# Kernel optimization log

Hardware: AMD Instinct MI355X
Metric: run time of the kernel (lower is better)

## Reference

```python
import jax, jax.numpy as jnp
import numpy as np

B, S, E = 2, 2048, 1024
H = 16
D = E // H  # 64
SCALE = D ** -0.5


def setup_inputs() -> dict:
    key = jax.random.key(0)
    ks = jax.random.split(key, 9)
    w = lambda k: jax.random.normal(k, (E, E), dtype=jnp.float32) * 0.02
    b = lambda k: jax.random.normal(k, (E,), dtype=jnp.float32) * 0.02
    return {
        "hidden_states": jax.random.normal(ks[0], (B, S, E), dtype=jnp.float32),
        "q_w": w(ks[1]), "q_b": b(ks[2]),
        "k_w": w(ks[3]), "k_b": b(ks[4]),
        "v_w": w(ks[5]), "v_b": b(ks[6]),
        "o_w": w(ks[7]), "o_b": b(ks[8]),
    }


def reference(hidden_states, q_w, q_b, k_w, k_b, v_w, v_b, o_w, o_b):
    dtype = hidden_states.dtype
    # torch Linear: y = x @ W^T + b
    q = hidden_states @ q_w.T + q_b
    k = hidden_states @ k_w.T + k_b
    v = hidden_states @ v_w.T + v_b
    # [B,S,E] -> [B*H, S, D]
    split = lambda t: t.reshape(B, S, H, D).transpose(0, 2, 1, 3).reshape(B * H, S, D)
    q, k, v = split(q), split(k), split(v)
    # upcast_attention: fp32 QK^T, scaled (baddbmm with beta=0, no mask)
    scores = SCALE * jnp.einsum("bqd,bkd->bqk", q.astype(jnp.float32), k.astype(jnp.float32))
    # upcast_softmax: fp32 softmax over last dim (transpose_qk=False), cast back
    probs = jax.nn.softmax(scores, axis=-1).astype(dtype)
    # PV bmm, merge heads, out_proj (dropout p=0.0 -> identity)
    out = jnp.einsum("bqk,bkd->bqd", probs, v)
    out = out.reshape(B, H, S, D).transpose(0, 2, 1, 3).reshape(B, S, E)
    return out @ o_w.T + o_b
```

## Files before the change

kernel.cpp:

```cpp
#include <hip/hip_runtime.h>

typedef __bf16 bf16x8 __attribute__((ext_vector_type(8)));
typedef __bf16 bf16x4 __attribute__((ext_vector_type(4)));
typedef float  f32x4  __attribute__((ext_vector_type(4)));

#define CS 0.18033688011112042f

__device__ __forceinline__ float fast_exp2(float x) {
    return __builtin_amdgcn_exp2f(x);
}

__device__ __forceinline__ f32x4 MFMA(bf16x8 a, bf16x8 b, f32x4 c) {
    return __builtin_amdgcn_mfma_f32_16x16x32_bf16(a, b, c, 0, 0, 0);
}

__device__ __forceinline__ void ldsgcpy16(__bf16* lds, const __bf16* g) {
    __builtin_amdgcn_global_load_lds(
        (const __attribute__((address_space(1))) unsigned int*)g,
        (__attribute__((address_space(3))) unsigned int*)lds, 16, 0, 0);
}

__global__ __launch_bounds__(256) void cvt5_kernel(
    const float* __restrict__ s0, const float* __restrict__ s1,
    const float* __restrict__ s2, const float* __restrict__ s3,
    const float* __restrict__ s4,
    __bf16* __restrict__ d0, __bf16* __restrict__ d1, __bf16* __restrict__ d2,
    __bf16* __restrict__ d3, __bf16* __restrict__ d4)
{
    int blk = blockIdx.x;
    const float* src; __bf16* dst; int base;
    if (blk < 4096)      { src = s0; dst = d0; base = blk; }
    else if (blk < 5120) { src = s1; dst = d1; base = blk - 4096; }
    else if (blk < 6144) { src = s2; dst = d2; base = blk - 5120; }
    else if (blk < 7168) { src = s3; dst = d3; base = blk - 6144; }
    else                 { src = s4; dst = d4; base = blk - 7168; }
    int i = base * 1024 + threadIdx.x * 4;
    float4 v = *(const float4*)(src + i);
    bf16x4 o;
    o[0] = (__bf16)v.x; o[1] = (__bf16)v.y; o[2] = (__bf16)v.z; o[3] = (__bf16)v.w;
    *(bf16x4*)(dst + i) = o;
}

template <typename OutT, int BN>
__device__ __forceinline__ void gemm_core(const __bf16* __restrict__ A,
                                          const __bf16* __restrict__ W,
                                          const float* __restrict__ bias,
                                          OutT* __restrict__ C,
                                          int m0, int n0, bool vtrans)
{
    constexpr int NJ = BN / 32;
    __shared__ __bf16 As[128 * 64];
    __shared__ __bf16 Bs[BN * 64];

    const int tid  = threadIdx.x;
    const int lane = tid & 63;
    const int w    = tid >> 6;
    const int wm   = w & 1;
    const int wn   = w >> 1;
    const int s    = lane & 15;
    const int q    = lane >> 4;

    f32x4 acc[4][NJ];
#pragma unroll
    for (int i = 0; i < 4; i++)
#pragma unroll
        for (int j = 0; j < NJ; j++)
#pragma unroll
            for (int r = 0; r < 4; r++) acc[i][j][r] = 0.0f;

    for (int k0 = 0; k0 < 1024; k0 += 64) {
        __syncthreads();
#pragma unroll
        for (int t = 0; t < 4; t++) {
            int c   = tid + 256 * t;
            int row = c >> 3;
            int ccp = (c & 7) ^ (row & 7);
            ldsgcpy16(&As[c * 8], A + (size_t)(m0 + row) * 1024 + k0 + ccp * 8);
        }
#pragma unroll
        for (int t = 0; t < BN / 32; t++) {
            int c   = tid + 256 * t;
            int row = c >> 3;
            int ccp = (c & 7) ^ (row & 7);
            ldsgcpy16(&Bs[c * 8], W + (size_t)(n0 + row) * 1024 + k0 + ccp * 8);
        }
        __syncthreads();

#pragma unroll
        for (int kk = 0; kk < 2; kk++) {
            bf16x8 af[4], bf[NJ];
#pragma unroll
            for (int i = 0; i < 4; i++) {
                int row = wm * 64 + i * 16 + s;
                int idx = row * 64 + ((((kk << 2) + q) ^ (row & 7)) << 3);
                af[i] = *(const bf16x8*)&As[idx];
            }
#pragma unroll
            for (int j = 0; j < NJ; j++) {
                int row = wn * (BN / 2) + j * 16 + s;
                int idx = row * 64 + ((((kk << 2) + q) ^ (row & 7)) << 3);
                bf[j] = *(const bf16x8*)&Bs[idx];
            }
#pragma unroll
            for (int i = 0; i < 4; i++)
#pragma unroll
                for (int j = 0; j < NJ; j++)
                    acc[i][j] = MFMA(af[i], bf[j], acc[i][j]);
        }
    }

    if (vtrans) {
        __bf16* Vt = (__bf16*)C;
#pragma unroll
        for (int j = 0; j < NJ; j++) {
            int col = n0 + wn * (BN / 2) + j * 16 + s;
            int h   = col >> 6;
            int d   = col & 63;
            float bv = bias[col];
#pragma unroll
            for (int i = 0; i < 4; i++) {
                int rowb = m0 + wm * 64 + i * 16 + q * 4;
                int b    = rowb >> 11;
                int srow = rowb & 2047;
                bf16x4 pk;
#pragma unroll
                for (int r = 0; r < 4; r++) pk[r] = (__bf16)(acc[i][j][r] + bv);
                *(bf16x4*)&Vt[(size_t)((b * 16 + h) * 64 + d) * 2048 + srow] = pk;
            }
        }
    } else {
#pragma unroll
        for (int j = 0; j < NJ; j++) {
            int col = n0 + wn * (BN / 2) + j * 16 + s;
            float bv = bias[col];
#pragma unroll
            for (int i = 0; i < 4; i++) {
                int rowb = m0 + wm * 64 + i * 16 + q * 4;
#pragma unroll
                for (int r = 0; r < 4; r++) {
                    C[(size_t)(rowb + r) * 1024 + col] = (OutT)(acc[i][j][r] + bv);
                }
            }
        }
    }
}

__global__ __launch_bounds__(256) void gemm_qkv_kernel(
    const __bf16* __restrict__ X,
    const __bf16* __restrict__ Wq, const float* __restrict__ bq,
    const __bf16* __restrict__ Wk, const float* __restrict__ bk,
    const __bf16* __restrict__ Wv, const float* __restrict__ bv,
    __bf16* __restrict__ Q, __bf16* __restrict__ K, __bf16* __restrict__ Vt)
{
    int mt = blockIdx.x / 24;
    int nt = blockIdx.x % 24;
    int which = nt >> 3;
    const __bf16* W    = (which == 0) ? Wq : (which == 1) ? Wk : Wv;
    const float*  bias = (which == 0) ? bq : (which == 1) ? bk : bv;
    __bf16*       Out  = (which == 0) ? Q  : (which == 1) ? K  : Vt;
    gemm_core<__bf16, 128>(X, W, bias, Out, mt * 128, (nt & 7) * 128, which == 2);
}

__global__ __launch_bounds__(256) void gemm_o_kernel(
    const __bf16* __restrict__ Ain, const __bf16* __restrict__ Wo,
    const float* __restrict__ bo, float* __restrict__ Out)
{
    int mt = blockIdx.x >> 4;
    int nt = blockIdx.x & 15;
    gemm_core<float, 64>(Ain, Wo, bo, Out, mt * 128, nt * 64, false);
}

__global__ __launch_bounds__(256, 2) void attn_kernel(
    const __bf16* __restrict__ Q, const __bf16* __restrict__ K,
    const __bf16* __restrict__ Vt, __bf16* __restrict__ O)
{
    __shared__ __bf16 k_lds[128 * 64];
    __shared__ __bf16 vt_lds[64 * 128];
    __shared__ __bf16 p_lds[4 * 32 * 128];

    const int bh = blockIdx.x >> 4;
    const int qt = blockIdx.x & 15;
    const int b  = bh >> 4;
    const int h  = bh & 15;

    const int tid  = threadIdx.x;
    const int lane = tid & 63;
    const int w    = tid >> 6;
    const int s    = lane & 15;
    const int q    = lane >> 4;

    bf16x8 aq[2][2];
#pragma unroll
    for (int i = 0; i < 2; i++)
#pragma unroll
        for (int kd = 0; kd < 2; kd++) {
            int row = qt * 128 + w * 32 + i * 16 + s;
            aq[i][kd] = *(const bf16x8*)(Q + (size_t)(b * 2048 + row) * 1024 +
                                         h * 64 + kd * 32 + q * 8);
        }

    f32x4 acc_o[2][4];
    float lst[2][4];
#pragma unroll
    for (int i = 0; i < 2; i++)
#pragma unroll
        for (int r = 0; r < 4; r++) {
            lst[i][r] = 0.0f;
#pragma unroll
            for (int jd = 0; jd < 4; jd++) acc_o[i][jd][r] = 0.0f;
        }

    const int pbase = w * 32 * 128;

    bf16x8 kpre[4], vpre[4];
#pragma unroll
    for (int t = 0; t < 4; t++) {
        int c = tid + 256 * t;
        int krow = c >> 3, cc = c & 7;
        kpre[t] = *(const bf16x8*)(K + (size_t)(b * 2048 + krow) * 1024 +
                                   h * 64 + cc * 8);
        int d = c >> 4, ck = c & 15;
        vpre[t] = *(const bf16x8*)(Vt + (size_t)(bh * 64 + d) * 2048 + ck * 8);
    }

    for (int kc = 0; kc < 16; kc++) {
        __syncthreads();
#pragma unroll
        for (int t = 0; t < 4; t++) {
            int c = tid + 256 * t;
            int krow = c >> 3, cc = c & 7;
            int rho  = ((krow & 7) << 4) | (krow >> 3);
            *(bf16x8*)&k_lds[rho * 64 + ((cc ^ (rho & 7)) << 3)] = kpre[t];
            int d = c >> 4, ck = c & 15;
            *(bf16x8*)&vt_lds[(d * 16 + (ck ^ (d & 7))) << 3] = vpre[t];
        }
        __syncthreads();

        int kb2 = ((kc + 1) & 15) * 128;
#pragma unroll
        for (int t = 0; t < 4; t++) {
            int c = tid + 256 * t;
            int krow = c >> 3, cc = c & 7;
            kpre[t] = *(const bf16x8*)(K + (size_t)(b * 2048 + kb2 + krow) * 1024 +
                                       h * 64 + cc * 8);
            int d = c >> 4, ck = c & 15;
            vpre[t] = *(const bf16x8*)(Vt + (size_t)(bh * 64 + d) * 2048 + kb2 + ck * 8);
        }

        f32x4 sc[2][8];
#pragma unroll
        for (int i = 0; i < 2; i++)
#pragma unroll
            for (int j = 0; j < 8; j++)
#pragma unroll
                for (int r = 0; r < 4; r++) sc[i][j][r] = 0.0f;
#pragma unroll
        for (int kd = 0; kd < 2; kd++) {
#pragma unroll
            for (int j = 0; j < 8; j++) {
                int row = j * 16 + s;
                int idx = row * 64 + ((((kd << 2) + q) ^ (row & 7)) << 3);
                bf16x8 bf = *(const bf16x8*)&k_lds[idx];
                sc[0][j] = MFMA(aq[0][kd], bf, sc[0][j]);
                sc[1][j] = MFMA(aq[1][kd], bf, sc[1][j]);
            }
        }

#pragma unroll
        for (int i = 0; i < 2; i++)
#pragma unroll
            for (int r = 0; r < 4; r++) {
                int prow = i * 16 + q * 4 + r;
                bf16x8 pk;
                float rsum = 0.0f;
#pragma unroll
                for (int j = 0; j < 8; j++) {
                    float p = fast_exp2(sc[i][j][r] * CS);
                    rsum += p;
                    pk[j] = (__bf16)p;
                }
                lst[i][r] += rsum;
                int chunkp = s ^ (prow & 15);
                *(bf16x8*)&p_lds[pbase + prow * 128 + (chunkp << 3)] = pk;
            }

#pragma unroll
        for (int kk = 0; kk < 4; kk++) {
            bf16x8 ap[2];
#pragma unroll
            for (int i = 0; i < 2; i++) {
                int prow = i * 16 + s;
                int chunkr = ((kk << 2) + q) ^ s;
                ap[i] = *(const bf16x8*)&p_lds[pbase + prow * 128 + (chunkr << 3)];
            }
#pragma unroll
            for (int jd = 0; jd < 4; jd++) {
                int d    = jd * 16 + s;
                int vidx = (d * 16 + (((kk << 2) + q) ^ (d & 7))) << 3;
                bf16x8 bv = *(const bf16x8*)&vt_lds[vidx];
                acc_o[0][jd] = MFMA(ap[0], bv, acc_o[0][jd]);
                acc_o[1][jd] = MFMA(ap[1], bv, acc_o[1][jd]);
            }
        }
    }

#pragma unroll
    for (int i = 0; i < 2; i++)
#pragma unroll
        for (int r = 0; r < 4; r++) {
#pragma unroll
            for (int off = 1; off < 16; off <<= 1)
                lst[i][r] += __shfl_xor(lst[i][r], off);
        }

#pragma unroll
    for (int i = 0; i < 2; i++)
#pragma unroll
        for (int jd = 0; jd < 4; jd++)
#pragma unroll
            for (int r = 0; r < 4; r++) {
                int row = qt * 128 + w * 32 + i * 16 + q * 4 + r;
                int col = h * 64 + jd * 16 + s;
                float v = acc_o[i][jd][r] / lst[i][r];
                O[(size_t)(b * 2048 + row) * 1024 + col] = (__bf16)v;
            }
}

extern "C" void kernel_launch(void* const* d_in, const int* in_sizes, int n_in,
                              void* d_out, int out_size, void* d_ws, size_t ws_size,
                              hipStream_t stream)
{
    const float* hs = (const float*)d_in[0];
    const float* qw = (const float*)d_in[1];
    const float* qb = (const float*)d_in[2];
    const float* kw = (const float*)d_in[3];
    const float* kb = (const float*)d_in[4];
    const float* vw = (const float*)d_in[5];
    const float* vb = (const float*)d_in[6];
    const float* ow = (const float*)d_in[7];
    const float* ob = (const float*)d_in[8];
    float* out = (float*)d_out;

    char* ws = (char*)d_ws;
    const size_t MB = (size_t)1024 * 1024;
    __bf16* Xb  = (__bf16*)(ws);
    __bf16* Wqb = (__bf16*)(ws +  8 * MB);
    __bf16* Wkb = (__bf16*)(ws + 10 * MB);
    __bf16* Wvb = (__bf16*)(ws + 12 * MB);
    __bf16* Wob = (__bf16*)(ws + 14 * MB);
    __bf16* Qb  = (__bf16*)(ws + 16 * MB);
    __bf16* Kb  = (__bf16*)(ws + 24 * MB);
    __bf16* Vtb = (__bf16*)(ws + 32 * MB);
    __bf16* Ab  = (__bf16*)(ws + 40 * MB);

    cvt5_kernel<<<dim3(8192), dim3(256), 0, stream>>>(hs, qw, kw, vw, ow,
                                                      Xb, Wqb, Wkb, Wvb, Wob);

    gemm_qkv_kernel<<<dim3(768), dim3(256), 0, stream>>>(Xb, Wqb, qb, Wkb, kb, Wvb, vb,
                                                         Qb, Kb, Vtb);
    attn_kernel<<<dim3(512), dim3(256), 0, stream>>>(Qb, Kb, Vtb, Ab);
    gemm_o_kernel<<<dim3(512), dim3(256), 0, stream>>>(Ab, Wob, ob, out);
}
```

Baseline: 201.0 us.

## Register-prefetch next GEMM K-tile and remap block order for weight reuse

Replaces direct global-to-LDS async copies in the GEMM core with register prefetch: the next K-tile is loaded into registers while the current tile is computed from LDS, then stored swizzled into LDS. It also changes the block-index mapping in the QKV and output GEMMs so consecutive blocks share the same weight column tile across M tiles. The aim is to hide global load latency and improve L2 reuse of weights, at the cost of extra VGPRs and explicit LDS stores.

```diff
diff --git a/kernel.cpp b/kernel.cpp
--- a/kernel.cpp
+++ b/kernel.cpp
@@ -12,12 +12,6 @@
 
 __device__ __forceinline__ f32x4 MFMA(bf16x8 a, bf16x8 b, f32x4 c) {
     return __builtin_amdgcn_mfma_f32_16x16x32_bf16(a, b, c, 0, 0, 0);
-}
-
-__device__ __forceinline__ void ldsgcpy16(__bf16* lds, const __bf16* g) {
-    __builtin_amdgcn_global_load_lds(
-        (const __attribute__((address_space(1))) unsigned int*)g,
-        (__attribute__((address_space(3))) unsigned int*)lds, 16, 0, 0);
 }
 
 __global__ __launch_bounds__(256) void cvt5_kernel(
@@ -68,23 +62,45 @@
 #pragma unroll
             for (int r = 0; r < 4; r++) acc[i][j][r] = 0.0f;
 
+    bf16x8 apre[4], bpre[NJ];
+#pragma unroll
+    for (int t = 0; t < 4; t++) {
+        int c = tid + 256 * t, row = c >> 3, cc = c & 7;
+        apre[t] = *(const bf16x8*)(A + (size_t)(m0 + row) * 1024 + cc * 8);
+    }
+#pragma unroll
+    for (int t = 0; t < NJ; t++) {
+        int c = tid + 256 * t, row = c >> 3, cc = c & 7;
+        bpre[t] = *(const bf16x8*)(W + (size_t)(n0 + row) * 1024 + cc * 8);
+    }
+
     for (int k0 = 0; k0 < 1024; k0 += 64) {
         __syncthreads();
 #pragma unroll
         for (int t = 0; t < 4; t++) {
-            int c   = tid + 256 * t;
-            int row = c >> 3;
-            int ccp = (c & 7) ^ (row & 7);
-            ldsgcpy16(&As[c * 8], A + (size_t)(m0 + row) * 1024 + k0 + ccp * 8);
-        }
-#pragma unroll
-        for (int t = 0; t < BN / 32; t++) {
-            int c   = tid + 256 * t;
-            int row = c >> 3;
-            int ccp = (c & 7) ^ (row & 7);
-            ldsgcpy16(&Bs[c * 8], W + (size_t)(n0 + row) * 1024 + k0 + ccp * 8);
+            int c = tid + 256 * t, row = c >> 3, cc = c & 7;
+            *(bf16x8*)&As[row * 64 + ((cc ^ (row & 7)) << 3)] = apre[t];
+        }
+#pragma unroll
+        for (int t = 0; t < NJ; t++) {
+            int c = tid + 256 * t, row = c >> 3, cc = c & 7;
+            *(bf16x8*)&Bs[row * 64 + ((cc ^ (row & 7)) << 3)] = bpre[t];
         }
         __syncthreads();
+
+        if (k0 < 1024 - 64) {
+            int kn = k0 + 64;
+#pragma unroll
+            for (int t = 0; t < 4; t++) {
+                int c = tid + 256 * t, row = c >> 3, cc = c & 7;
+                apre[t] = *(const bf16x8*)(A + (size_t)(m0 + row) * 1024 + kn + cc * 8);
+            }
+#pragma unroll
+            for (int t = 0; t < NJ; t++) {
+                int c = tid + 256 * t, row = c >> 3, cc = c & 7;
+                bpre[t] = *(const bf16x8*)(W + (size_t)(n0 + row) * 1024 + kn + cc * 8);
+            }
+        }
 
 #pragma unroll
         for (int kk = 0; kk < 2; kk++) {
@@ -152,21 +168,21 @@
     const __bf16* __restrict__ Wv, const float* __restrict__ bv,
     __bf16* __restrict__ Q, __bf16* __restrict__ K, __bf16* __restrict__ Vt)
 {
-    int mt = blockIdx.x / 24;
-    int nt = blockIdx.x % 24;
-    int which = nt >> 3;
+    int mt   = blockIdx.x & 31;
+    int ntot = blockIdx.x >> 5;
+    int which = ntot >> 3;
     const __bf16* W    = (which == 0) ? Wq : (which == 1) ? Wk : Wv;
     const float*  bias = (which == 0) ? bq : (which == 1) ? bk : bv;
     __bf16*       Out  = (which == 0) ? Q  : (which == 1) ? K  : Vt;
-    gemm_core<__bf16, 128>(X, W, bias, Out, mt * 128, (nt & 7) * 128, which == 2);
+    gemm_core<__bf16, 128>(X, W, bias, Out, mt * 128, (ntot & 7) * 128, which == 2);
 }
 
 __global__ __launch_bounds__(256) void gemm_o_kernel(
     const __bf16* __restrict__ Ain, const __bf16* __restrict__ Wo,
     const float* __restrict__ bo, float* __restrict__ Out)
 {
-    int mt = blockIdx.x >> 4;
-    int nt = blockIdx.x & 15;
+    int mt = blockIdx.x & 31;
+    int nt = blockIdx.x >> 5;
     gemm_core<float, 64>(Ain, Wo, bo, Out, mt * 128, nt * 64, false);
 }
 
```

Result: faster. 188.4 us (-6.3%).
